# Kernel tuning notes

Measured on AMD Instinct MI355X. Metric: run time of the kernel, lower is better.

## Reference

```python
import jax, jax.numpy as jnp
from jax import lax
import numpy as np

T, B, I, H = 365, 2048, 9, 50


def setup_inputs() -> dict:
    key = jax.random.key(0)
    ks = jax.random.split(key, 12)
    s = 0.1
    return {
        "x": jax.random.normal(ks[0], (T, B, I), dtype=jnp.float32),
        "w_ih0": jax.random.normal(ks[1], (4 * H, I), dtype=jnp.float32) * s,
        "w_hh0": jax.random.normal(ks[2], (4 * H, H), dtype=jnp.float32) * s,
        "b_ih0": jax.random.normal(ks[3], (4 * H,), dtype=jnp.float32) * s,
        "b_hh0": jax.random.normal(ks[4], (4 * H,), dtype=jnp.float32) * s,
        "w_ih1": jax.random.normal(ks[5], (4 * H, H), dtype=jnp.float32) * s,
        "w_hh1": jax.random.normal(ks[6], (4 * H, H), dtype=jnp.float32) * s,
        "b_ih1": jax.random.normal(ks[7], (4 * H,), dtype=jnp.float32) * s,
        "b_hh1": jax.random.normal(ks[8], (4 * H,), dtype=jnp.float32) * s,
        "fc_w": jax.random.normal(ks[9], (1, H), dtype=jnp.float32) * s,
        "fc_b": jax.random.normal(ks[10], (1,), dtype=jnp.float32) * s,
    }


def _lstm_layer(x, w_ih, w_hh, b_ih, b_hh):
    # x: [T, B, in]; PyTorch gate order: i, f, g, o
    Bq = x.shape[1]
    Hh = w_hh.shape[1]
    # precompute input projections for all timesteps (one big GEMM)
    x_proj = jnp.einsum('tbi,gi->tbg', x, w_ih) + b_ih + b_hh  # [T, B, 4H]

    def step(carry, xp):
        h, c = carry
        gates = xp + h @ w_hh.T  # [B, 4H]
        i, f, g, o = jnp.split(gates, 4, axis=-1)
        i = jax.nn.sigmoid(i)
        f = jax.nn.sigmoid(f)
        g = jnp.tanh(g)
        o = jax.nn.sigmoid(o)
        c = f * c + i * g
        h = o * jnp.tanh(c)
        return (h, c), h

    h0 = jnp.zeros((Bq, Hh), dtype=x.dtype)
    _, hs = lax.scan(step, (h0, h0), x_proj)
    return hs  # [T, B, H]


def reference(x, w_ih0, w_hh0, b_ih0, b_hh0, w_ih1, w_hh1, b_ih1, b_hh1, fc_w, fc_b):
    h1 = _lstm_layer(x, w_ih0, w_hh0, b_ih0, b_hh0)
    h2 = _lstm_layer(h1, w_ih1, w_hh1, b_ih1, b_hh1)
    out = jnp.einsum('tbh,oh->tbo', h2, fc_w) + fc_b  # [T, B, 1]
    return out
```

## Files before the change

kernel.cpp:

```cpp
#include <hip/hip_runtime.h>

#define T_STEPS 365
#define BATCH   2048
#define INP     9
#define HID     50
#define MB      16
#define NBLK    (BATCH/MB)
#define NT      1024
#define NTILES  13
#define TPW     2

typedef __attribute__((ext_vector_type(8))) short short8;
typedef __attribute__((ext_vector_type(4))) float float4v;

__device__ __forceinline__ unsigned short f2bf(float v) {
    unsigned u = __builtin_bit_cast(unsigned, v);
    unsigned r = (u + 0x7FFFu + ((u >> 16) & 1u)) >> 16;
    return (unsigned short)r;
}
__device__ __forceinline__ float sig_(float x) {
    return __builtin_amdgcn_rcpf(1.f + __expf(-x));
}
__device__ __forceinline__ float tanh_(float x) {
    return 1.f - 2.f * __builtin_amdgcn_rcpf(__expf(2.f * x) + 1.f);
}

__device__ __forceinline__ int hx_off(int m, int k) {
    return (m * 128 + k) ^ ((m & 7) << 3);
}

__global__ __launch_bounds__(NT, 4)
void lstm_pipe16(const float* __restrict__ x,
                 const float* __restrict__ w_ih0, const float* __restrict__ w_hh0,
                 const float* __restrict__ b_ih0, const float* __restrict__ b_hh0,
                 const float* __restrict__ w_ih1, const float* __restrict__ w_hh1,
                 const float* __restrict__ b_ih1, const float* __restrict__ b_hh1,
                 const float* __restrict__ fc_w, const float* __restrict__ fc_b,
                 float* __restrict__ out)
{
    __shared__ __align__(16) unsigned short HX[2][MB * 128];
    __shared__ float FCP[2][8][MB];

    const int t    = threadIdx.x;
    const int w    = t >> 6;
    const int lid  = t & 63;
    const int mcol = lid & 15;
    const int kgrp = lid >> 4;
    const int kb8  = kgrp * 8;
    const int b0   = blockIdx.x * MB;
    const bool isL1 = (w < 8);
    const int v    = w & 7;
    const float fcb = fc_b[0];

    short8 wA[TPW][4];
    float  bs[TPW][4], fcw[TPW], cst[TPW];
    const float* bih = isL1 ? b_ih1 : b_ih0;
    const float* bhh = isL1 ? b_hh1 : b_hh0;

    #pragma unroll
    for (int tt = 0; tt < TPW; ++tt) {
        const int T  = v + 8 * tt;
        const bool tv = (T < NTILES);
        const int r  = T * 16 + mcol;
        const bool rv = tv && (r < 4 * HID);
        const int u_r = r >> 2, g_r = r & 3;
        const int orig = g_r * HID + u_r;
        #pragma unroll
        for (int kt = 0; kt < 4; ++kt) {
            short8 f;
            #pragma unroll
            for (int j = 0; j < 8; ++j) {
                int k = kt * 32 + kb8 + j;
                float val = 0.f;
                if (rv) {
                    if (isL1) {
                        if (k < HID)                      val = w_ih1[orig * HID + k];
                        else if (k >= 64 && k < 64 + HID) val = w_hh1[orig * HID + (k - 64)];
                    } else {
                        if (k < HID)            val = w_hh0[orig * HID + k];
                        else if (k < HID + INP) val = w_ih0[orig * INP + (k - HID)];
                    }
                }
                f[j] = (short)f2bf(val);
            }
            wA[tt][kt] = f;
        }
        const int u_lane = T * 4 + kgrp;
        #pragma unroll
        for (int rr = 0; rr < 4; ++rr) {
            int row = T * 16 + kgrp * 4 + rr;
            bool bvv = tv && (row < 4 * HID);
            int uu = row >> 2;
            bs[tt][rr] = bvv ? (bih[rr * HID + uu] + bhh[rr * HID + uu]) : 0.f;
        }
        fcw[tt] = (isL1 && tv && u_lane < HID) ? fc_w[u_lane] : 0.f;
        cst[tt] = 0.f;
    }

    int xi = -1;
    if (w == 8) xi = lid;
    else if (w == 9) xi = 64 + lid;
    else if (w == 10 && lid < 16) xi = 128 + lid;
    const bool xact = (xi >= 0 && xi < MB * INP);
    const int xm = xact ? xi / INP : 0, xj = xact ? xi % INP : 0;

    for (int i = t; i < 2 * MB * 128; i += NT) (&HX[0][0])[i] = 0;
    if (t < 2 * 8 * MB) (&FCP[0][0][0])[t] = 0.f;
    __syncthreads();
    float xreg = 0.f;
    if (xact) {
        HX[1][hx_off(xm, HID + xj)] = f2bf(x[(size_t)(b0 + xm) * INP + xj]);
        xreg = x[((size_t)BATCH + b0 + xm) * INP + xj];
    }
    __syncthreads();

    for (int ph = 0; ph < T_STEPS + 2; ++ph) {
        const int cur = (ph + 1) & 1, nxt = ph & 1;

        short8 f0 = *(const short8*)&HX[cur][hx_off(mcol, kb8)];
        short8 f1 = *(const short8*)&HX[cur][hx_off(mcol, 32 + kb8)];

        if (isL1) {
            if (ph >= 1 && ph <= T_STEPS) {
                short8 f2 = *(const short8*)&HX[cur][hx_off(mcol, 64 + kb8)];
                short8 f3 = *(const short8*)&HX[cur][hx_off(mcol, 96 + kb8)];
                float h1v[TPW];
                float fcp = 0.f;
                #pragma unroll
                for (int tt = 0; tt < TPW; ++tt) {
                    const int T = v + 8 * tt;
                    if (T < NTILES) {
                        float4v accA = {bs[tt][0], bs[tt][1], bs[tt][2], bs[tt][3]};
                        float4v accB = {0.f, 0.f, 0.f, 0.f};
                        accA = __builtin_amdgcn_mfma_f32_16x16x32_bf16(wA[tt][0], f0, accA, 0, 0, 0);
                        accB = __builtin_amdgcn_mfma_f32_16x16x32_bf16(wA[tt][2], f2, accB, 0, 0, 0);
                        accA = __builtin_amdgcn_mfma_f32_16x16x32_bf16(wA[tt][1], f1, accA, 0, 0, 0);
                        accB = __builtin_amdgcn_mfma_f32_16x16x32_bf16(wA[tt][3], f3, accB, 0, 0, 0);
                        float a0 = accA[0] + accB[0], a1 = accA[1] + accB[1];
                        float a2 = accA[2] + accB[2], a3 = accA[3] + accB[3];
                        float gi = sig_(a0), gf = sig_(a1);
                        float gg = tanh_(a2), go = sig_(a3);
                        cst[tt] = gf * cst[tt] + gi * gg;
                        h1v[tt] = go * tanh_(cst[tt]);
                        fcp += fcw[tt] * h1v[tt];
                    }
                }
                #pragma unroll
                for (int tt = 0; tt < TPW; ++tt) {
                    const int T = v + 8 * tt, u = T * 4 + kgrp;
                    if (T < NTILES && u < HID)
                        HX[nxt][hx_off(mcol, 64 + u)] = f2bf(h1v[tt]);
                }
                fcp += __shfl_xor(fcp, 16);
                fcp += __shfl_xor(fcp, 32);
                if (lid < MB) FCP[ph & 1][v][lid] = fcp;
            }
        } else {
            if (ph < T_STEPS) {
                float h0v[TPW];
                #pragma unroll
                for (int tt = 0; tt < TPW; ++tt) {
                    const int T = v + 8 * tt;
                    if (T < NTILES) {
                        float4v acc = {bs[tt][0], bs[tt][1], bs[tt][2], bs[tt][3]};
                        acc = __builtin_amdgcn_mfma_f32_16x16x32_bf16(wA[tt][0], f0, acc, 0, 0, 0);
                        acc = __builtin_amdgcn_mfma_f32_16x16x32_bf16(wA[tt][1], f1, acc, 0, 0, 0);
                        float gi = sig_(acc[0]), gf = sig_(acc[1]);
                        float gg = tanh_(acc[2]), go = sig_(acc[3]);
                        cst[tt] = gf * cst[tt] + gi * gg;
                        h0v[tt] = go * tanh_(cst[tt]);
                    }
                }
                #pragma unroll
                for (int tt = 0; tt < TPW; ++tt) {
                    const int T = v + 8 * tt, u = T * 4 + kgrp;
                    if (T < NTILES && u < HID)
                        HX[nxt][hx_off(mcol, u)] = f2bf(h0v[tt]);
                }
            }
            if (xact) {
                if (ph + 1 < T_STEPS) HX[nxt][hx_off(xm, HID + xj)] = f2bf(xreg);
                if (ph + 2 < T_STEPS) xreg = x[((size_t)(ph + 2) * BATCH + b0 + xm) * INP + xj];
            }
            if (w == 15 && lid < MB && ph >= 2) {
                const int rp = (ph - 1) & 1;
                float s = fcb;
                #pragma unroll
                for (int ww = 0; ww < 8; ++ww) s += FCP[rp][ww][lid];
                out[(size_t)(ph - 2) * BATCH + b0 + lid] = s;
            }
        }
        __syncthreads();
    }
}

extern "C" void kernel_launch(void* const* d_in, const int* in_sizes, int n_in,
                              void* d_out, int out_size, void* d_ws, size_t ws_size,
                              hipStream_t stream) {
    const float* x     = (const float*)d_in[0];
    const float* w_ih0 = (const float*)d_in[1];
    const float* w_hh0 = (const float*)d_in[2];
    const float* b_ih0 = (const float*)d_in[3];
    const float* b_hh0 = (const float*)d_in[4];
    const float* w_ih1 = (const float*)d_in[5];
    const float* w_hh1 = (const float*)d_in[6];
    const float* b_ih1 = (const float*)d_in[7];
    const float* b_hh1 = (const float*)d_in[8];
    const float* fc_w  = (const float*)d_in[9];
    const float* fc_b  = (const float*)d_in[10];
    float* out = (float*)d_out;

    lstm_pipe16<<<dim3(NBLK), dim3(NT), 0, stream>>>(
        x, w_ih0, w_hh0, b_ih0, b_hh0,
        w_ih1, w_hh1, b_ih1, b_hh1, fc_w, fc_b, out);
}
```

Measured before the change: 354.2 us.

## Fold exp2 scaling into weights, prefetch x early, and use lighter phase barrier

Pre-scales the LSTM weights and biases by -log2(e) (doubled for the g gate) so each gate activation becomes a raw exp2 plus a reciprocal, with no per-step multiply and no exp-to-exp2 conversion. The global load of x is moved to the top of each phase so its latency overlaps the MFMA work. __syncthreads is replaced by a custom barrier that waits only on LDS counters and adds a scheduling fence, which removes the wait on outstanding global memory operations. Folding the scale in before bf16 rounding slightly changes numerics, and the custom barrier relies on the global loads and stores not needing ordering at the barrier.

```diff
diff --git a/kernel.cpp b/kernel.cpp
--- a/kernel.cpp
+++ b/kernel.cpp
@@ -10,6 +10,8 @@
 #define NTILES  13
 #define TPW     2
 
+#define L2E     1.4426950408889634f
+
 typedef __attribute__((ext_vector_type(8))) short short8;
 typedef __attribute__((ext_vector_type(4))) float float4v;
 
@@ -18,25 +20,25 @@
     unsigned r = (u + 0x7FFFu + ((u >> 16) & 1u)) >> 16;
     return (unsigned short)r;
 }
-__device__ __forceinline__ float sig_(float x) {
-    return __builtin_amdgcn_rcpf(1.f + __expf(-x));
-}
-__device__ __forceinline__ float tanh_(float x) {
-    return 1.f - 2.f * __builtin_amdgcn_rcpf(__expf(2.f * x) + 1.f);
-}
+
+#define PHASE_BARRIER() do {                                  \
+    asm volatile("s_waitcnt lgkmcnt(0)" ::: "memory");        \
+    __builtin_amdgcn_s_barrier();                             \
+    __builtin_amdgcn_sched_barrier(0);                        \
+} while (0)
 
 __device__ __forceinline__ int hx_off(int m, int k) {
     return (m * 128 + k) ^ ((m & 7) << 3);
 }
 
 __global__ __launch_bounds__(NT, 4)
-void lstm_pipe16(const float* __restrict__ x,
-                 const float* __restrict__ w_ih0, const float* __restrict__ w_hh0,
-                 const float* __restrict__ b_ih0, const float* __restrict__ b_hh0,
-                 const float* __restrict__ w_ih1, const float* __restrict__ w_hh1,
-                 const float* __restrict__ b_ih1, const float* __restrict__ b_hh1,
-                 const float* __restrict__ fc_w, const float* __restrict__ fc_b,
-                 float* __restrict__ out)
+void lstm_pipe16b(const float* __restrict__ x,
+                  const float* __restrict__ w_ih0, const float* __restrict__ w_hh0,
+                  const float* __restrict__ b_ih0, const float* __restrict__ b_hh0,
+                  const float* __restrict__ w_ih1, const float* __restrict__ w_hh1,
+                  const float* __restrict__ b_ih1, const float* __restrict__ b_hh1,
+                  const float* __restrict__ fc_w, const float* __restrict__ fc_b,
+                  float* __restrict__ out)
 {
     __shared__ __align__(16) unsigned short HX[2][MB * 128];
     __shared__ float FCP[2][8][MB];
@@ -65,6 +67,7 @@
         const bool rv = tv && (r < 4 * HID);
         const int u_r = r >> 2, g_r = r & 3;
         const int orig = g_r * HID + u_r;
+        const float rsc = (g_r == 2) ? (-2.f * L2E) : (-L2E);
         #pragma unroll
         for (int kt = 0; kt < 4; ++kt) {
             short8 f;
@@ -81,7 +84,7 @@
                         else if (k < HID + INP) val = w_ih0[orig * INP + (k - HID)];
                     }
                 }
-                f[j] = (short)f2bf(val);
+                f[j] = (short)f2bf(val * rsc);
             }
             wA[tt][kt] = f;
         }
@@ -91,7 +94,8 @@
             int row = T * 16 + kgrp * 4 + rr;
             bool bvv = tv && (row < 4 * HID);
             int uu = row >> 2;
-            bs[tt][rr] = bvv ? (bih[rr * HID + uu] + bhh[rr * HID + uu]) : 0.f;
+            const float bsc = (rr == 2) ? (-2.f * L2E) : (-L2E);
+            bs[tt][rr] = bvv ? (bih[rr * HID + uu] + bhh[rr * HID + uu]) * bsc : 0.f;
         }
         fcw[tt] = (isL1 && tv && u_lane < HID) ? fc_w[u_lane] : 0.f;
         cst[tt] = 0.f;
@@ -117,6 +121,10 @@
     for (int ph = 0; ph < T_STEPS + 2; ++ph) {
         const int cur = (ph + 1) & 1, nxt = ph & 1;
 
+        float xnew = 0.f;
+        if (xact && ph + 2 < T_STEPS)
+            xnew = x[((size_t)(ph + 2) * BATCH + b0 + xm) * INP + xj];
+
         short8 f0 = *(const short8*)&HX[cur][hx_off(mcol, kb8)];
         short8 f1 = *(const short8*)&HX[cur][hx_off(mcol, 32 + kb8)];
 
@@ -136,12 +144,19 @@
                         accB = __builtin_amdgcn_mfma_f32_16x16x32_bf16(wA[tt][2], f2, accB, 0, 0, 0);
                         accA = __builtin_amdgcn_mfma_f32_16x16x32_bf16(wA[tt][1], f1, accA, 0, 0, 0);
                         accB = __builtin_amdgcn_mfma_f32_16x16x32_bf16(wA[tt][3], f3, accB, 0, 0, 0);
-                        float a0 = accA[0] + accB[0], a1 = accA[1] + accB[1];
-                        float a2 = accA[2] + accB[2], a3 = accA[3] + accB[3];
-                        float gi = sig_(a0), gf = sig_(a1);
-                        float gg = tanh_(a2), go = sig_(a3);
+                        float Ei = __builtin_amdgcn_exp2f(accA[0] + accB[0]);
+                        float Ef = __builtin_amdgcn_exp2f(accA[1] + accB[1]);
+                        float Eg = __builtin_amdgcn_exp2f(accA[2] + accB[2]);
+                        float Eo = __builtin_amdgcn_exp2f(accA[3] + accB[3]);
+                        float gi = __builtin_amdgcn_rcpf(1.f + Ei);
+                        float gf = __builtin_amdgcn_rcpf(1.f + Ef);
+                        float g2 = __builtin_amdgcn_rcpf(1.f + Eg);
+                        float go = __builtin_amdgcn_rcpf(1.f + Eo);
+                        float gg = __builtin_fmaf(2.f, g2, -1.f);
                         cst[tt] = gf * cst[tt] + gi * gg;
-                        h1v[tt] = go * tanh_(cst[tt]);
+                        float Ec = __builtin_amdgcn_exp2f(cst[tt] * (-2.f * L2E));
+                        float tc = __builtin_fmaf(2.f, __builtin_amdgcn_rcpf(1.f + Ec), -1.f);
+                        h1v[tt] = go * tc;
                         fcp += fcw[tt] * h1v[tt];
                     }
                 }
@@ -165,10 +180,19 @@
                         float4v acc = {bs[tt][0], bs[tt][1], bs[tt][2], bs[tt][3]};
                         acc = __builtin_amdgcn_mfma_f32_16x16x32_bf16(wA[tt][0], f0, acc, 0, 0, 0);
                         acc = __builtin_amdgcn_mfma_f32_16x16x32_bf16(wA[tt][1], f1, acc, 0, 0, 0);
-                        float gi = sig_(acc[0]), gf = sig_(acc[1]);
-                        float gg = tanh_(acc[2]), go = sig_(acc[3]);
+                        float Ei = __builtin_amdgcn_exp2f(acc[0]);
+                        float Ef = __builtin_amdgcn_exp2f(acc[1]);
+                        float Eg = __builtin_amdgcn_exp2f(acc[2]);
+                        float Eo = __builtin_amdgcn_exp2f(acc[3]);
+                        float gi = __builtin_amdgcn_rcpf(1.f + Ei);
+                        float gf = __builtin_amdgcn_rcpf(1.f + Ef);
+                        float g2 = __builtin_amdgcn_rcpf(1.f + Eg);
+                        float go = __builtin_amdgcn_rcpf(1.f + Eo);
+                        float gg = __builtin_fmaf(2.f, g2, -1.f);
                         cst[tt] = gf * cst[tt] + gi * gg;
-                        h0v[tt] = go * tanh_(cst[tt]);
+                        float Ec = __builtin_amdgcn_exp2f(cst[tt] * (-2.f * L2E));
+                        float tc = __builtin_fmaf(2.f, __builtin_amdgcn_rcpf(1.f + Ec), -1.f);
+                        h0v[tt] = go * tc;
                     }
                 }
                 #pragma unroll
@@ -178,10 +202,8 @@
                         HX[nxt][hx_off(mcol, u)] = f2bf(h0v[tt]);
                 }
             }
-            if (xact) {
-                if (ph + 1 < T_STEPS) HX[nxt][hx_off(xm, HID + xj)] = f2bf(xreg);
-                if (ph + 2 < T_STEPS) xreg = x[((size_t)(ph + 2) * BATCH + b0 + xm) * INP + xj];
-            }
+            if (xact && ph + 1 < T_STEPS)
+                HX[nxt][hx_off(xm, HID + xj)] = f2bf(xreg);
             if (w == 15 && lid < MB && ph >= 2) {
                 const int rp = (ph - 1) & 1;
                 float s = fcb;
@@ -190,7 +212,8 @@
                 out[(size_t)(ph - 2) * BATCH + b0 + lid] = s;
             }
         }
-        __syncthreads();
+        xreg = xnew;
+        PHASE_BARRIER();
     }
 }
 
@@ -210,7 +233,7 @@
     const float* fc_b  = (const float*)d_in[10];
     float* out = (float*)d_out;
 
-    lstm_pipe16<<<dim3(NBLK), dim3(NT), 0, stream>>>(
+    lstm_pipe16b<<<dim3(NBLK), dim3(NT), 0, stream>>>(
         x, w_ih0, w_hh0, b_ih0, b_hh0,
         w_ih1, w_hh1, b_ih1, b_hh1, fc_w, fc_b, out);
 }
```

Measured after the change: 349.2 us. No clear change (-1.4%).
